# Kernel tuning notes

Measured on AMD Instinct MI355X. Metric: run time of the kernel, lower is better.

Reference implementation:

```python
import jax, jax.numpy as jnp
import numpy as np

N_EMBD = 1024
N_HEAD = 16
HEAD_DIM = N_EMBD // N_HEAD
INNER = 4 * N_EMBD
EPS = 1e-5


def setup_inputs() -> dict:
    key = jax.random.key(0)
    ks = jax.random.split(key, 13)
    s = lambda d: 1.0 / np.sqrt(d)
    return {
        "x": jax.random.normal(ks[0], (2, 2048, N_EMBD), jnp.float32),
        "ln1_g": jnp.ones((N_EMBD,), jnp.float32),
        "ln1_b": jnp.zeros((N_EMBD,), jnp.float32),
        "w_attn": jax.random.normal(ks[1], (N_EMBD, 3 * N_EMBD), jnp.float32) * s(N_EMBD),
        "b_attn": jnp.zeros((3 * N_EMBD,), jnp.float32),
        "w_proj": jax.random.normal(ks[2], (N_EMBD, N_EMBD), jnp.float32) * s(N_EMBD),
        "b_proj": jnp.zeros((N_EMBD,), jnp.float32),
        "ln2_g": jnp.ones((N_EMBD,), jnp.float32),
        "ln2_b": jnp.zeros((N_EMBD,), jnp.float32),
        "w_fc": jax.random.normal(ks[3], (N_EMBD, INNER), jnp.float32) * s(N_EMBD),
        "b_fc": jnp.zeros((INNER,), jnp.float32),
        "w_fc2": jax.random.normal(ks[4], (INNER, N_EMBD), jnp.float32) * s(INNER),
        "b_fc2": jnpp if False else jnp.zeros((N_EMBD,), jnp.float32),
    }


def _layernorm(x, g, b):
    mu = jnp.mean(x, axis=-1, keepdims=True)
    var = jnp.mean(jnp.square(x - mu), axis=-1, keepdims=True)
    return (x - mu) * jax.lax.rsqrt(var + EPS) * g + b


def _attention(x, w_attn, b_attn, w_proj, b_proj):
    B, T, C = x.shape
    qkv = x @ w_attn + b_attn                      # [B,T,3C]
    q, k, v = jnp.split(qkv, 3, axis=-1)
    q = q.reshape(B, T, N_HEAD, HEAD_DIM).transpose(0, 2, 1, 3)  # [B,H,T,D]
    k = k.reshape(B, T, N_HEAD, HEAD_DIM).transpose(0, 2, 1, 3)
    v = v.reshape(B, T, N_HEAD, HEAD_DIM).transpose(0, 2, 1, 3)
    scale = HEAD_DIM ** -0.5
    scores = jnp.einsum("bhqd,bhkd->bhqk", q, k) * scale         # [B,H,T,T]
    causal = jnp.triu(jnp.ones((T, T), jnp.bool_), k=1)
    scores = jnp.where(causal, -jnp.inf, scores)
    attn = jax.nn.softmax(scores, axis=-1)
    out = jnp.einsum("bhqk,bhkd->bhqd", attn, v)                 # [B,H,T,D]
    out = out.transpose(0, 2, 1, 3).reshape(B, T, C)
    return out @ w_proj + b_proj


def reference(x, ln1_g, ln1_b, w_attn, b_attn, w_proj, b_proj,
              ln2_g, ln2_b, w_fc, b_fc, w_fc2, b_fc2):
    h = x + _attention(_layernorm(x, ln1_g, ln1_b), w_attn, b_attn, w_proj, b_proj)
    m = _layernorm(h, ln2_g, ln2_b)
    m = jax.nn.gelu(m @ w_fc + b_fc, approximate=False) @ w_fc2 + b_fc2
    return h + m
```

## Files before the change

kernel.cpp:

```cpp
#include <hip/hip_runtime.h>

typedef unsigned short u16;
typedef unsigned int u32;
typedef short v8s __attribute__((ext_vector_type(8)));
typedef short v4s __attribute__((ext_vector_type(4)));
typedef float v4f __attribute__((ext_vector_type(4)));

__device__ __forceinline__ float b2f(u16 v) {
    return __uint_as_float(((u32)v) << 16);
}
__device__ __forceinline__ u16 f2b(float f) {
    u32 u = __float_as_uint(f);
    return (u16)((u + 0x7FFFu + ((u >> 16) & 1u)) >> 16);
}
__device__ __forceinline__ v4f mfma16(v8s a, v8s b, v4f c) {
    return __builtin_amdgcn_mfma_f32_16x16x32_bf16(a, b, c, 0, 0, 0);
}

__device__ __forceinline__ void gload_lds16(const u16* g, u16* l) {
    __builtin_amdgcn_global_load_lds((const __attribute__((address_space(1))) void*)g,
                                     (__attribute__((address_space(3))) void*)l, 16, 0, 0);
}

__global__ void detect_k(const void* x, int* flag) {
    __shared__ int cnt;
    if (threadIdx.x == 0) cnt = 0;
    __syncthreads();
    const u16* p = (const u16*)x;
    int bad = 0;
    for (int i = threadIdx.x; i < 4096; i += 256) {
        int e = (p[i] >> 7) & 0xFF;
        if (e != 0 && (e < 100 || e > 140)) bad++;
    }
    atomicAdd(&cnt, bad);
    __syncthreads();
    if (threadIdx.x == 0) *flag = (cnt > 256) ? 1 : 0;
}

__global__ void cvt_k(const void* __restrict__ src, u16* __restrict__ dst, int n,
                      const int* __restrict__ flag) {
    const int isf32 = *flag;
    for (int i = blockIdx.x * 256 + threadIdx.x; i < n; i += gridDim.x * 256)
        dst[i] = isf32 ? f2b(((const float*)src)[i]) : ((const u16*)src)[i];
}

struct P8 { const void* p[8]; };
__global__ void cvt_small_k(P8 src, u16* __restrict__ bb, const int* __restrict__ flag) {
    const int isf32 = *flag;
    const int len[8] = {3072, 1024, 4096, 1024, 1024, 1024, 1024, 1024};
    const int doff[8] = {0, 4096, 8192, 12288, 16384, 17408, 18432, 19456};
    int gi = blockIdx.x * 256 + threadIdx.x;
    int seg = 0, off = gi;
    while (seg < 7 && off >= len[seg]) { off -= len[seg]; seg++; }
    if (off < len[seg]) {
        const void* s = src.p[seg];
        bb[doff[seg] + off] = isf32 ? f2b(((const float*)s)[off]) : ((const u16*)s)[off];
    }
}

__global__ void transpose_k(const void* __restrict__ in, u16* __restrict__ out, int R, int C,
                            const int* __restrict__ flag) {
    __shared__ u16 t[32][33];
    const int isf32 = *flag;
    const int c0 = blockIdx.x * 32, r0 = blockIdx.y * 32;
    for (int i = threadIdx.y; i < 32; i += 8) {
        size_t idx = (size_t)(r0 + i) * C + c0 + threadIdx.x;
        t[i][threadIdx.x] = isf32 ? f2b(((const float*)in)[idx]) : ((const u16*)in)[idx];
    }
    __syncthreads();
    for (int i = threadIdx.y; i < 32; i += 8)
        out[(size_t)(c0 + i) * R + r0 + threadIdx.x] = t[threadIdx.x][i];
}

__global__ __launch_bounds__(256) void layernorm_k(const u16* __restrict__ x,
                                                   const u16* __restrict__ g,
                                                   const u16* __restrict__ bta,
                                                   u16* __restrict__ out) {
    const int wid = threadIdx.x >> 6, lane = threadIdx.x & 63;
    const size_t row = (size_t)blockIdx.x * 4 + wid;
    const u16* xr = x + row * 1024 + lane * 16;
    u16 v[16];
    *(uint4*)&v[0] = *(const uint4*)xr;
    *(uint4*)&v[8] = *(const uint4*)(xr + 8);
    float f[16], s = 0.f, sq = 0.f;
#pragma unroll
    for (int i = 0; i < 16; i++) { f[i] = b2f(v[i]); s += f[i]; sq += f[i] * f[i]; }
#pragma unroll
    for (int d = 1; d < 64; d <<= 1) { s += __shfl_xor(s, d, 64); sq += __shfl_xor(sq, d, 64); }
    const float mean = s * (1.f / 1024.f);
    const float var = sq * (1.f / 1024.f) - mean * mean;
    const float rstd = rsqrtf(var + 1e-5f);
    u16 gv[16], bv[16];
    *(uint4*)&gv[0] = *(const uint4*)(g + lane * 16);
    *(uint4*)&gv[8] = *(const uint4*)(g + lane * 16 + 8);
    *(uint4*)&bv[0] = *(const uint4*)(bta + lane * 16);
    *(uint4*)&bv[8] = *(const uint4*)(bta + lane * 16 + 8);
    u16 ov[16];
#pragma unroll
    for (int i = 0; i < 16; i++) ov[i] = f2b((f[i] - mean) * rstd * b2f(gv[i]) + b2f(bv[i]));
    u16* orow = out + row * 1024 + lane * 16;
    *(uint4*)orow = *(uint4*)&ov[0];
    *(uint4*)(orow + 8) = *(uint4*)&ov[8];
}

#define GEMM_STAGE(tk, buf)                                              \
    do {                                                                 \
        const int _k = (tk) << 5;                                        \
        gload_lds16(Ag + _k, &As[buf][0] + wid * 512);                   \
        gload_lds16(Ag + (size_t)64 * K + _k, &As[buf][2048] + wid * 512); \
        gload_lds16(Bg + _k, &Bs[buf][0] + wid * 512);                   \
        gload_lds16(Bg + (size_t)64 * K + _k, &Bs[buf][2048] + wid * 512); \
    } while (0)

__global__ __launch_bounds__(256) void gemm_bt_k(const u16* __restrict__ A,
                                                 const u16* __restrict__ Bt,
                                                 const u16* __restrict__ bias,
                                                 const u16* __restrict__ res,
                                                 void* __restrict__ C,
                                                 int M, int N, int K, int do_gelu,
                                                 const int* __restrict__ outf32) {
    __shared__ __align__(16) u16 As[3][4096];
    __shared__ __align__(16) u16 Bs[3][4096];
    const int tid = threadIdx.x;
    const int wid = tid >> 6, lane = tid & 63;
    const int lg = lane >> 4, lm = lane & 15;
    const int wr = wid >> 1, wc = wid & 1;
    const int nwg = gridDim.x * gridDim.y;
    const int orig = blockIdx.y * gridDim.x + blockIdx.x;
    const int wg = (orig & 7) * (nwg >> 3) + (orig >> 3);
    const int m0 = (wg / gridDim.x) * 128, n0 = (wg % gridDim.x) * 128;

    const v4f vzero = {0.f, 0.f, 0.f, 0.f};
    v4f acc[4][4];
#pragma unroll
    for (int i = 0; i < 4; i++)
#pragma unroll
        for (int j = 0; j < 4; j++) acc[i][j] = vzero;

    const int srow = tid >> 2;
    const int scol = (((tid & 3) ^ ((tid >> 3) & 3)) * 8);
    const u16* Ag = A + (size_t)(m0 + srow) * K + scol;
    const u16* Bg = Bt + (size_t)(n0 + srow) * K + scol;
    const int lgx = (lg ^ ((lm >> 1) & 3)) * 8;

    const int nt = K >> 5;
    GEMM_STAGE(0, 0);
    GEMM_STAGE(1, 1);
    for (int t = 0; t < nt; ++t) {
        const int cur = t % 3;
        if (t + 2 < nt) {
            GEMM_STAGE(t + 2, (t + 2) % 3);
            asm volatile("s_waitcnt vmcnt(8)" ::: "memory");
        } else if (t + 1 < nt) {
            asm volatile("s_waitcnt vmcnt(4)" ::: "memory");
        } else {
            asm volatile("s_waitcnt vmcnt(0)" ::: "memory");
        }
        __builtin_amdgcn_s_barrier();
        v8s af[4], bf[4];
#pragma unroll
        for (int i = 0; i < 4; i++)
            af[i] = *(const v8s*)&As[cur][(wr * 64 + i * 16 + lm) * 32 + lgx];
#pragma unroll
        for (int j = 0; j < 4; j++)
            bf[j] = *(const v8s*)&Bs[cur][(wc * 64 + j * 16 + lm) * 32 + lgx];
        __builtin_amdgcn_s_setprio(1);
#pragma unroll
        for (int i = 0; i < 4; i++)
#pragma unroll
            for (int j = 0; j < 4; j++)
                acc[i][j] = __builtin_amdgcn_mfma_f32_16x16x32_bf16(af[i], bf[j], acc[i][j], 0, 0, 0);
        __builtin_amdgcn_s_setprio(0);
        asm volatile("s_waitcnt lgkmcnt(0)" ::: "memory");
        __builtin_amdgcn_sched_barrier(0);
        __builtin_amdgcn_s_barrier();
    }

    const int of32 = outf32 ? *outf32 : 0;
#pragma unroll
    for (int i = 0; i < 4; i++) {
#pragma unroll
        for (int r = 0; r < 4; r++) {
            const int row = m0 + wr * 64 + i * 16 + lg * 4 + r;
            const size_t rb = (size_t)row * N;
#pragma unroll
            for (int j = 0; j < 4; j++) {
                const int col = n0 + wc * 64 + j * 16 + lm;
                float v = acc[i][j][r] + b2f(bias[col]);
                if (do_gelu) v = 0.5f * v * (1.0f + erff(v * 0.70710678118f));
                if (res) v += b2f(res[rb + col]);
                if (of32) ((float*)C)[rb + col] = v;
                else ((u16*)C)[rb + col] = f2b(v);
            }
        }
    }
}

#define ST256(LDSARR, P, tt, h)                                                  \
    do {                                                                         \
        const u16* _s = (P) + (size_t)((h) * 128) * K + (size_t)(tt) * 64;       \
        gload_lds16(_s, &LDSARR[(tt) & 1][h][0] + wv * 512);                     \
        gload_lds16(_s + (size_t)64 * K, &LDSARR[(tt) & 1][h][4096] + wv * 512); \
    } while (0)

#define MMROW(ii, x0, x1)                                   \
    acc[ii][0] = mfma16(x0, bfr[0][0], acc[ii][0]);         \
    acc[ii][0] = mfma16(x1, bfr[0][1], acc[ii][0]);         \
    acc[ii][1] = mfma16(x0, bfr[1][0], acc[ii][1]);         \
    acc[ii][1] = mfma16(x1, bfr[1][1], acc[ii][1]);         \
    acc[ii][2] = mfma16(x0, bfr[2][0], acc[ii][2]);         \
    acc[ii][2] = mfma16(x1, bfr[2][1], acc[ii][2]);         \
    acc[ii][3] = mfma16(x0, bfr[3][0], acc[ii][3]);         \
    acc[ii][3] = mfma16(x1, bfr[3][1], acc[ii][3]);

#define RD_A2(i0, i1)                                         \
    x0 = *(const v8s*)(ABase + (i0) * 1024 + offk0);          \
    x1 = *(const v8s*)(ABase + (i0) * 1024 + offk1);          \
    y0 = *(const v8s*)(ABase + (i1) * 1024 + offk0);          \
    y1 = *(const v8s*)(ABase + (i1) * 1024 + offk1);

__global__ __launch_bounds__(512, 2) void gemm256_k(const u16* __restrict__ A,
                                                    const u16* __restrict__ Bt,
                                                    const u16* __restrict__ bias,
                                                    const u16* __restrict__ res,
                                                    void* __restrict__ C,
                                                    int M, int N, int K, int do_gelu,
                                                    const int* __restrict__ outf32) {
    __shared__ __align__(16) u16 As[2][2][8192];
    __shared__ __align__(16) u16 Bs[2][2][8192];
    const int tid = threadIdx.x;
    const int wv = tid >> 6, lane = tid & 63;
    const int lg = lane >> 4, lm = lane & 15;
    const int wm = wv >> 2, wn = wv & 3;
    const int nwg = gridDim.x * gridDim.y;
    const int orig = blockIdx.y * gridDim.x + blockIdx.x;
    const int wg = (orig & 7) * (nwg >> 3) + (orig >> 3);
    const int m0 = (wg / gridDim.x) * 256, n0 = (wg % gridDim.x) * 256;

    const v4f vzero = {0.f, 0.f, 0.f, 0.f};
    v4f acc[8][4];
#pragma unroll
    for (int i = 0; i < 8; i++)
#pragma unroll
        for (int j = 0; j < 4; j++) acc[i][j] = vzero;

    const int trow = tid >> 3;
    const int csw = ((tid & 7) ^ (trow & 7)) * 8;
    const u16* Ap = A + (size_t)(m0 + trow) * K + csw;
    const u16* Bp = Bt + (size_t)(n0 + trow) * K + csw;
    const int offk0 = lm * 64 + ((lg ^ (lm & 7)) << 3);
    const int offk1 = offk0 ^ 32;

    const int NT = K >> 6;
    ST256(As, Ap, 0, 0); ST256(As, Ap, 0, 1);
    ST256(Bs, Bp, 0, 0); ST256(Bs, Bp, 0, 1);
    ST256(Bs, Bp, 1, 0); ST256(Bs, Bp, 1, 1);
    asm volatile("s_waitcnt vmcnt(4)" ::: "memory");
    __builtin_amdgcn_s_barrier();

    for (int t = 0; t < NT; ++t) {
        const int d = t & 1;
        const u16* ABase = &As[d][wm][0];
        const u16* BBase = &Bs[d][wn >> 1][(wn & 1) * 4096];
        v8s bfr[4][2];
        v8s x0, x1, y0, y1;
#pragma unroll
        for (int j = 0; j < 4; j++) {
            bfr[j][0] = *(const v8s*)(BBase + j * 1024 + offk0);
            bfr[j][1] = *(const v8s*)(BBase + j * 1024 + offk1);
        }
        RD_A2(0, 1)
        if (t + 1 < NT) { ST256(As, Ap, t + 1, 0); }
        __builtin_amdgcn_s_barrier();
        asm volatile("s_waitcnt lgkmcnt(0)" ::: "memory");
        __builtin_amdgcn_s_setprio(1);
        MMROW(0, x0, x1)
        MMROW(1, y0, y1)
        __builtin_amdgcn_s_setprio(0);
        __builtin_amdgcn_s_barrier();
        RD_A2(2, 3)
        if (t + 1 < NT) { ST256(As, Ap, t + 1, 1); }
        __builtin_amdgcn_s_barrier();
        asm volatile("s_waitcnt lgkmcnt(0)" ::: "memory");
        __builtin_amdgcn_s_setprio(1);
        MMROW(2, x0, x1)
        MMROW(3, y0, y1)
        __builtin_amdgcn_s_setprio(0);
        __builtin_amdgcn_s_barrier();
        RD_A2(4, 5)
        if (t + 2 < NT) { ST256(Bs, Bp, t + 2, 0); }
        __builtin_amdgcn_s_barrier();
        asm volatile("s_waitcnt lgkmcnt(0)" ::: "memory");
        __builtin_amdgcn_s_setprio(1);
        MMROW(4, x0, x1)
        MMROW(5, y0, y1)
        __builtin_amdgcn_s_setprio(0);
        __builtin_amdgcn_s_barrier();
        RD_A2(6, 7)
        if (t + 2 < NT) {
            ST256(Bs, Bp, t + 2, 1);
            asm volatile("s_waitcnt vmcnt(4)" ::: "memory");
        } else {
            asm volatile("s_waitcnt vmcnt(0)" ::: "memory");
        }
        __builtin_amdgcn_s_barrier();
        asm volatile("s_waitcnt lgkmcnt(0)" ::: "memory");
        __builtin_amdgcn_s_setprio(1);
        MMROW(6, x0, x1)
        MMROW(7, y0, y1)
        __builtin_amdgcn_s_setprio(0);
        __builtin_amdgcn_s_barrier();
    }

    const int of32 = outf32 ? *outf32 : 0;
#pragma unroll
    for (int i = 0; i < 8; i++) {
#pragma unroll
        for (int r = 0; r < 4; r++) {
            const int row = m0 + wm * 128 + i * 16 + lg * 4 + r;
            const size_t rb = (size_t)row * N;
#pragma unroll
            for (int j = 0; j < 4; j++) {
                const int col = n0 + wn * 64 + j * 16 + lm;
                float v = acc[i][j][r] + b2f(bias[col]);
                if (do_gelu) v = 0.5f * v * (1.0f + erff(v * 0.70710678118f));
                if (res) v += b2f(res[rb + col]);
                if (of32) ((float*)C)[rb + col] = v;
                else ((u16*)C)[rb + col] = f2b(v);
            }
        }
    }
}

__global__ __launch_bounds__(256) void gemm_qkv_k(const u16* __restrict__ A,
                                                  const u16* __restrict__ Bt,
                                                  const u16* __restrict__ bias,
                                                  u16* __restrict__ Qh,
                                                  u16* __restrict__ Kh,
                                                  u16* __restrict__ Vth) {
    __shared__ __align__(16) u16 As[3][4096];
    __shared__ __align__(16) u16 Bs[3][4096];
    const int tid = threadIdx.x;
    const int wid = tid >> 6, lane = tid & 63;
    const int lg = lane >> 4, lm = lane & 15;
    const int wr = wid >> 1, wc = wid & 1;
    const int nwg = gridDim.x * gridDim.y;
    const int orig = blockIdx.y * gridDim.x + blockIdx.x;
    const int wg = (orig & 7) * (nwg >> 3) + (orig >> 3);
    const int m0 = (wg / gridDim.x) * 128, n0 = (wg % gridDim.x) * 128;
    const int K = 1024;

    const v4f vzero = {0.f, 0.f, 0.f, 0.f};
    v4f acc[4][4];
#pragma unroll
    for (int i = 0; i < 4; i++)
#pragma unroll
        for (int j = 0; j < 4; j++) acc[i][j] = vzero;

    const int srow = tid >> 2;
    const int scol = (((tid & 3) ^ ((tid >> 3) & 3)) * 8);
    const u16* Ag = A + (size_t)(m0 + srow) * K + scol;
    const u16* Bg = Bt + (size_t)(n0 + srow) * K + scol;
    const int lgx = (lg ^ ((lm >> 1) & 3)) * 8;

    const int nt = K >> 5;
    GEMM_STAGE(0, 0);
    GEMM_STAGE(1, 1);
    for (int t = 0; t < nt; ++t) {
        const int cur = t % 3;
        if (t + 2 < nt) {
            GEMM_STAGE(t + 2, (t + 2) % 3);
            asm volatile("s_waitcnt vmcnt(8)" ::: "memory");
        } else if (t + 1 < nt) {
            asm volatile("s_waitcnt vmcnt(4)" ::: "memory");
        } else {
            asm volatile("s_waitcnt vmcnt(0)" ::: "memory");
        }
        __builtin_amdgcn_s_barrier();
        v8s af[4], bf[4];
#pragma unroll
        for (int i = 0; i < 4; i++)
            af[i] = *(const v8s*)&As[cur][(wr * 64 + i * 16 + lm) * 32 + lgx];
#pragma unroll
        for (int j = 0; j < 4; j++)
            bf[j] = *(const v8s*)&Bs[cur][(wc * 64 + j * 16 + lm) * 32 + lgx];
        __builtin_amdgcn_s_setprio(1);
#pragma unroll
        for (int i = 0; i < 4; i++)
#pragma unroll
            for (int j = 0; j < 4; j++)
                acc[i][j] = __builtin_amdgcn_mfma_f32_16x16x32_bf16(af[i], bf[j], acc[i][j], 0, 0, 0);
        __builtin_amdgcn_s_setprio(0);
        asm volatile("s_waitcnt lgkmcnt(0)" ::: "memory");
        __builtin_amdgcn_sched_barrier(0);
        __builtin_amdgcn_s_barrier();
    }

    const int which = n0 >> 10;
    const int h = ((n0 & 1023) >> 6) + wc;
    if (which < 2) {
        u16* dst = which ? Kh : Qh;
        const float qsc = which ? 1.0f : 0.18033688011f;
#pragma unroll
        for (int i = 0; i < 4; i++) {
#pragma unroll
            for (int r = 0; r < 4; r++) {
                const int row = m0 + wr * 64 + i * 16 + lg * 4 + r;
                const int b = row >> 11, t = row & 2047;
                const size_t rb = ((size_t)(b * 16 + h) * 2048 + t) * 64;
#pragma unroll
                for (int j = 0; j < 4; j++) {
                    float v = (acc[i][j][r] + b2f(bias[n0 + wc * 64 + j * 16 + lm])) * qsc;
                    dst[rb + j * 16 + lm] = f2b(v);
                }
            }
        }
    } else {
#pragma unroll
        for (int i = 0; i < 4; i++) {
            const int t0 = m0 + wr * 64 + i * 16 + lg * 4;
            const int b = t0 >> 11, tt = t0 & 2047;
            const int w = tt & 31;
            const int pos = (tt & ~31) + ((w & 15) >> 2) * 8 + ((w >> 4) & 1) * 4;
#pragma unroll
            for (int j = 0; j < 4; j++) {
                const int d = j * 16 + lm;
                const float bv_ = b2f(bias[n0 + wc * 64 + j * 16 + lm]);
                u16 pk[4];
#pragma unroll
                for (int r = 0; r < 4; r++) pk[r] = f2b(acc[i][j][r] + bv_);
                *(v4s*)&Vth[((size_t)(b * 16 + h) * 64 + d) * 2048 + pos] = *(const v4s*)pk;
            }
        }
    }
}

__global__ __launch_bounds__(256, 4) void attn10_k(const u16* __restrict__ Qh,
                                                   const u16* __restrict__ Kh,
                                                   const u16* __restrict__ Vth,
                                                   u16* __restrict__ out) {
    __shared__ __align__(16) u16 Ks[2][4096];
    __shared__ __align__(16) u16 Vs[2][4096];
    const int tid = threadIdx.x;
    const int wid = tid >> 6, lane = tid & 63;
    const int lg = lane >> 4, lm = lane & 15;
    const int i = blockIdx.x;
    const int q = i >> 8, s = i & 255;
    const int bh = s & 31;
    const int g8 = s >> 5;
    const int g = (q == 0) ? g8 : (q == 1) ? (15 - g8) : (q == 2) ? (16 + g8) : (31 - g8);
    const int q0 = g * 64 + wid * 16;
    const int qrow_l = q0 + lm;
    const size_t qkb = (size_t)bh * 2048;
    const v4f vzero = {0.f, 0.f, 0.f, 0.f};
    const int nch = g + 1;

    const int r0 = tid >> 3;
    const int colp = ((tid & 7) * 16) ^ ((r0 & 7) << 4);
    const u16* Ksrc0 = Kh + (qkb + r0) * 64 + (colp >> 1);
    const u16* Ksrc1 = Ksrc0 + 32 * 64;
    const u16* Vsrc0 = Vth + ((size_t)bh * 64 + r0) * 2048 + (colp >> 1);
    const u16* Vsrc1 = Vsrc0 + (size_t)32 * 2048;
    const int wslot = wid * 512;

    const int xorv = (lm & 7) << 4;
    const int ro1 = (lm * 128 + ((lg * 16) ^ xorv)) >> 1;
    const int ro2 = (lm * 128 + (((lg * 16) + 64) ^ xorv)) >> 1;

    v8s aq[2];
    {
        const u16* qp = Qh + (qkb + q0 + lm) * 64 + lg * 8;
        aq[0] = *(const v8s*)qp;
        aq[1] = *(const v8s*)(qp + 32);
    }
    float l_run = 0.f;
    v4f o[4];
#pragma unroll
    for (int dt = 0; dt < 4; dt++) o[dt] = vzero;

    gload_lds16(Ksrc0, &Ks[0][0] + wslot);
    gload_lds16(Ksrc1, &Ks[0][2048] + wslot);
    gload_lds16(Vsrc0, &Vs[0][0] + wslot);
    gload_lds16(Vsrc1, &Vs[0][2048] + wslot);

    for (int ci = 0; ci < nch; ++ci) {
        const int cur = ci & 1;
        if (ci + 1 < nch) {
            const u16* kc = Ksrc0 + (ci + 1) * 4096;
            const u16* vc = Vsrc0 + (ci + 1) * 64;
            gload_lds16(kc, &Ks[cur ^ 1][0] + wslot);
            gload_lds16(kc + 32 * 64, &Ks[cur ^ 1][2048] + wslot);
            gload_lds16(vc, &Vs[cur ^ 1][0] + wslot);
            gload_lds16(vc + (size_t)32 * 2048, &Vs[cur ^ 1][2048] + wslot);
            asm volatile("s_waitcnt vmcnt(4)" ::: "memory");
        } else {
            asm volatile("s_waitcnt vmcnt(0)" ::: "memory");
        }
        __builtin_amdgcn_s_barrier();

        const u16* KB = &Ks[cur][0];
        const u16* VB = &Vs[cur][0];
        const int k0 = ci << 6;
        v4f sacc[4];
        __builtin_amdgcn_s_setprio(1);
#pragma unroll
        for (int kt = 0; kt < 4; kt++) {
            v8s klo = *(const v8s*)(KB + kt * 1024 + ro1);
            v8s khi = *(const v8s*)(KB + kt * 1024 + ro2);
            sacc[kt] = __builtin_amdgcn_mfma_f32_16x16x32_bf16(klo, aq[0], vzero, 0, 0, 0);
            sacc[kt] = __builtin_amdgcn_mfma_f32_16x16x32_bf16(khi, aq[1], sacc[kt], 0, 0, 0);
        }
        __builtin_amdgcn_s_setprio(0);
        float p[16];
        if (ci == nch - 1) {
#pragma unroll
            for (int kt = 0; kt < 4; kt++)
#pragma unroll
                for (int r = 0; r < 4; r++) {
                    float v = sacc[kt][r];
                    v = (k0 + kt * 16 + lg * 4 + r > qrow_l) ? -200.f : v;
                    p[kt * 4 + r] = exp2f(v);
                }
        } else {
#pragma unroll
            for (int kt = 0; kt < 4; kt++)
#pragma unroll
                for (int r = 0; r < 4; r++) p[kt * 4 + r] = exp2f(sacc[kt][r]);
        }
        float ls = 0.f;
#pragma unroll
        for (int e = 0; e < 16; e++) ls += p[e];
        l_run += ls;
        u32 pk[8];
#pragma unroll
        for (int j = 0; j < 8; j++) {
            u32 lo = __float_as_uint(p[j * 2]) + 0x8000u;
            u32 hi = __float_as_uint(p[j * 2 + 1]) + 0x8000u;
            pk[j] = __builtin_amdgcn_perm(hi, lo, 0x07060302u);
        }
        v8s B0, B1;
        ((u32*)&B0)[0] = pk[0]; ((u32*)&B0)[1] = pk[1];
        ((u32*)&B0)[2] = pk[2]; ((u32*)&B0)[3] = pk[3];
        ((u32*)&B1)[0] = pk[4]; ((u32*)&B1)[1] = pk[5];
        ((u32*)&B1)[2] = pk[6]; ((u32*)&B1)[3] = pk[7];
        __builtin_amdgcn_s_setprio(1);
#pragma unroll
        for (int dt = 0; dt < 4; dt++) {
            v8s vlo = *(const v8s*)(VB + dt * 1024 + ro1);
            v8s vhi = *(const v8s*)(VB + dt * 1024 + ro2);
            o[dt] = __builtin_amdgcn_mfma_f32_16x16x32_bf16(vlo, B0, o[dt], 0, 0, 0);
            o[dt] = __builtin_amdgcn_mfma_f32_16x16x32_bf16(vhi, B1, o[dt], 0, 0, 0);
        }
        __builtin_amdgcn_s_setprio(0);
        asm volatile("s_waitcnt lgkmcnt(0)" ::: "memory");
        __builtin_amdgcn_sched_barrier(0);
        __builtin_amdgcn_s_barrier();
    }
    l_run += __shfl_xor(l_run, 16, 64);
    l_run += __shfl_xor(l_run, 32, 64);
    const int b = bh >> 4, h = bh & 15;
    const float inv = 1.0f / l_run;
    const size_t rowb = ((size_t)b * 2048 + q0 + lm) * 1024 + h * 64;
#pragma unroll
    for (int dt = 0; dt < 4; dt++) {
        u16 pk2[4];
#pragma unroll
        for (int r = 0; r < 4; r++) pk2[r] = f2b(o[dt][r] * inv);
        *(v4s*)&out[rowb + dt * 16 + lg * 4] = *(const v4s*)pk2;
    }
}

extern "C" void kernel_launch(void* const* d_in, const int* in_sizes, int n_in,
                              void* d_out, int out_size, void* d_ws, size_t ws_size,
                              hipStream_t stream) {
    const void* x      = d_in[0];
    const void* ln1_g  = d_in[1];
    const void* ln1_b  = d_in[2];
    const void* w_attn = d_in[3];
    const void* b_attn = d_in[4];
    const void* w_proj = d_in[5];
    const void* b_proj = d_in[6];
    const void* ln2_g  = d_in[7];
    const void* ln2_b  = d_in[8];
    const void* w_fc   = d_in[9];
    const void* b_fc   = d_in[10];
    const void* w_fc2  = d_in[11];
    const void* b_fc2  = d_in[12];

    u16* ws = (u16*)d_ws;
    const size_t Mi = 1u << 20;
    u16* xb       = ws;
    u16* ln_buf   = ws + 4 * Mi;
    u16* h_buf    = ws + 8 * Mi;
    u16* wT_attn  = ws + 12 * Mi;
    u16* wT_proj  = ws + 15 * Mi;
    u16* wT_fc    = ws + 16 * Mi;
    u16* wT_fc2   = ws + 20 * Mi;
    u16* bb       = ws + 24 * Mi;
    u16* bb_attn = bb, *bb_proj = bb + 4096, *bb_fc = bb + 8192, *bb_fc2 = bb + 12288;
    u16* gsmall   = bb + 16384;
    u16* g_ln1g = gsmall, *g_ln1b = gsmall + 1024, *g_ln2g = gsmall + 2048, *g_ln2b = gsmall + 3072;
    int* flag     = (int*)(bb + 24576);
    u16* Qh       = ws + 25 * Mi;
    u16* Kh       = ws + 29 * Mi;
    u16* Vth      = ws + 33 * Mi;
    u16* attn_buf = ws + 37 * Mi;
    u16* fc_buf   = ws + 25 * Mi;

    detect_k<<<1, 256, 0, stream>>>(x, flag);

    cvt_k<<<4096, 256, 0, stream>>>(x, xb, 4 * Mi, flag);
    P8 smalls;
    smalls.p[0] = b_attn; smalls.p[1] = b_proj; smalls.p[2] = b_fc; smalls.p[3] = b_fc2;
    smalls.p[4] = ln1_g;  smalls.p[5] = ln1_b;  smalls.p[6] = ln2_g; smalls.p[7] = ln2_b;
    cvt_small_k<<<52, 256, 0, stream>>>(smalls, bb, flag);

    dim3 tb(32, 8);
    transpose_k<<<dim3(96, 32), tb, 0, stream>>>(w_attn, wT_attn, 1024, 3072, flag);
    transpose_k<<<dim3(32, 32), tb, 0, stream>>>(w_proj, wT_proj, 1024, 1024, flag);
    transpose_k<<<dim3(128, 32), tb, 0, stream>>>(w_fc, wT_fc, 1024, 4096, flag);
    transpose_k<<<dim3(32, 128), tb, 0, stream>>>(w_fc2, wT_fc2, 4096, 1024, flag);

    layernorm_k<<<1024, 256, 0, stream>>>(xb, g_ln1g, g_ln1b, ln_buf);
    gemm_qkv_k<<<dim3(24, 32), 256, 0, stream>>>(ln_buf, wT_attn, bb_attn, Qh, Kh, Vth);
    attn10_k<<<1024, 256, 0, stream>>>(Qh, Kh, Vth, attn_buf);
    gemm_bt_k<<<dim3(8, 32), 256, 0, stream>>>(attn_buf, wT_proj, bb_proj, xb, h_buf,
                                               4096, 1024, 1024, 0, nullptr);
    layernorm_k<<<1024, 256, 0, stream>>>(h_buf, g_ln2g, g_ln2b, ln_buf);
    gemm256_k<<<dim3(16, 16), 512, 0, stream>>>(ln_buf, wT_fc, bb_fc, nullptr, fc_buf,
                                                4096, 4096, 1024, 1, nullptr);
    gemm_bt_k<<<dim3(8, 32), 256, 0, stream>>>(fc_buf, wT_fc2, bb_fc2, h_buf, d_out,
                                               4096, 1024, 4096, 0, flag);
}
```

Baseline: 455.1 us.

## Split-K the FC2 GEMM into two fp32 partials with a fused reduce epilogue

Replaces the single FC2 GEMM launch (256 tiles with full K=4096) with a split-K kernel that runs 512 workgroups, each covering half of K with a 3-stage LDS pipeline. Each half writes fp32 partial results into reused workspace regions. A separate reduce kernel then adds the two partials, the bias and the residual, and writes the output in fp32 or bf16. The aim is more workgroups per CU for better latency hiding. The cost is extra fp32 partial traffic and one more kernel launch.

```diff
diff --git a/kernel.cpp b/kernel.cpp
--- a/kernel.cpp
+++ b/kernel.cpp
@@ -193,6 +193,111 @@
                 else ((u16*)C)[rb + col] = f2b(v);
             }
         }
+    }
+}
+
+__global__ __launch_bounds__(256) void gemm_sk_k(const u16* __restrict__ A,
+                                                 const u16* __restrict__ Bt,
+                                                 float* __restrict__ P0,
+                                                 float* __restrict__ P1,
+                                                 int N, int K) {
+    __shared__ __align__(16) u16 As[3][4096];
+    __shared__ __align__(16) u16 Bs[3][4096];
+    const int tid = threadIdx.x;
+    const int wid = tid >> 6, lane = tid & 63;
+    const int lg = lane >> 4, lm = lane & 15;
+    const int wr = wid >> 1, wc = wid & 1;
+    const int z = blockIdx.z;
+    const int KS = K >> 1;
+    const int nwg = gridDim.x * gridDim.y;
+    const int orig = blockIdx.y * gridDim.x + blockIdx.x;
+    const int wg = (orig & 7) * (nwg >> 3) + (orig >> 3);
+    const int m0 = (wg / gridDim.x) * 128, n0 = (wg % gridDim.x) * 128;
+
+    const v4f vzero = {0.f, 0.f, 0.f, 0.f};
+    v4f acc[4][4];
+#pragma unroll
+    for (int i = 0; i < 4; i++)
+#pragma unroll
+        for (int j = 0; j < 4; j++) acc[i][j] = vzero;
+
+    const int srow = tid >> 2;
+    const int scol = (((tid & 3) ^ ((tid >> 3) & 3)) * 8);
+    const u16* Ag = A + (size_t)(m0 + srow) * K + z * KS + scol;
+    const u16* Bg = Bt + (size_t)(n0 + srow) * K + z * KS + scol;
+    const int lgx = (lg ^ ((lm >> 1) & 3)) * 8;
+
+    const int nt = KS >> 5;
+    GEMM_STAGE(0, 0);
+    GEMM_STAGE(1, 1);
+    for (int t = 0; t < nt; ++t) {
+        const int cur = t % 3;
+        if (t + 2 < nt) {
+            GEMM_STAGE(t + 2, (t + 2) % 3);
+            asm volatile("s_waitcnt vmcnt(8)" ::: "memory");
+        } else if (t + 1 < nt) {
+            asm volatile("s_waitcnt vmcnt(4)" ::: "memory");
+        } else {
+            asm volatile("s_waitcnt vmcnt(0)" ::: "memory");
+        }
+        __builtin_amdgcn_s_barrier();
+        v8s af[4], bf[4];
+#pragma unroll
+        for (int i = 0; i < 4; i++)
+            af[i] = *(const v8s*)&As[cur][(wr * 64 + i * 16 + lm) * 32 + lgx];
+#pragma unroll
+        for (int j = 0; j < 4; j++)
+            bf[j] = *(const v8s*)&Bs[cur][(wc * 64 + j * 16 + lm) * 32 + lgx];
+        __builtin_amdgcn_s_setprio(1);
+#pragma unroll
+        for (int i = 0; i < 4; i++)
+#pragma unroll
+            for (int j = 0; j < 4; j++)
+                acc[i][j] = __builtin_amdgcn_mfma_f32_16x16x32_bf16(af[i], bf[j], acc[i][j], 0, 0, 0);
+        __builtin_amdgcn_s_setprio(0);
+        asm volatile("s_waitcnt lgkmcnt(0)" ::: "memory");
+        __builtin_amdgcn_sched_barrier(0);
+        __builtin_amdgcn_s_barrier();
+    }
+
+    float* P = z ? P1 : P0;
+#pragma unroll
+    for (int i = 0; i < 4; i++) {
+#pragma unroll
+        for (int r = 0; r < 4; r++) {
+            const int row = m0 + wr * 64 + i * 16 + lg * 4 + r;
+            const size_t rb = (size_t)row * N;
+#pragma unroll
+            for (int j = 0; j < 4; j++) {
+                const int col = n0 + wc * 64 + j * 16 + lm;
+                P[rb + col] = acc[i][j][r];
+            }
+        }
+    }
+}
+
+__global__ __launch_bounds__(256) void fc2red_k(const float* __restrict__ P0,
+                                                const float* __restrict__ P1,
+                                                const u16* __restrict__ bias,
+                                                const u16* __restrict__ res,
+                                                void* __restrict__ out,
+                                                const int* __restrict__ outf32) {
+    const int i = (blockIdx.x * 256 + threadIdx.x) * 4;
+    const int col = i & 1023;
+    float4 a = *(const float4*)(P0 + i);
+    float4 b = *(const float4*)(P1 + i);
+    v4s rv = *(const v4s*)(res + i);
+    v4s bv = *(const v4s*)(bias + col);
+    float v0 = a.x + b.x + b2f(bv[0]) + b2f(rv[0]);
+    float v1 = a.y + b.y + b2f(bv[1]) + b2f(rv[1]);
+    float v2 = a.z + b.z + b2f(bv[2]) + b2f(rv[2]);
+    float v3 = a.w + b.w + b2f(bv[3]) + b2f(rv[3]);
+    if (*outf32) {
+        float4 o = {v0, v1, v2, v3};
+        *(float4*)((float*)out + i) = o;
+    } else {
+        u16 pk[4] = {f2b(v0), f2b(v1), f2b(v2), f2b(v3)};
+        *(v4s*)((u16*)out + i) = *(const v4s*)pk;
     }
 }
 
@@ -606,6 +711,8 @@
     u16* Vth      = ws + 33 * Mi;
     u16* attn_buf = ws + 37 * Mi;
     u16* fc_buf   = ws + 25 * Mi;
+    float* P0f    = (float*)ws;
+    float* P1f    = (float*)(ws + 12 * Mi);
 
     detect_k<<<1, 256, 0, stream>>>(x, flag);
 
@@ -629,6 +736,6 @@
     layernorm_k<<<1024, 256, 0, stream>>>(h_buf, g_ln2g, g_ln2b, ln_buf);
     gemm256_k<<<dim3(16, 16), 512, 0, stream>>>(ln_buf, wT_fc, bb_fc, nullptr, fc_buf,
                                                 4096, 4096, 1024, 1, nullptr);
-    gemm_bt_k<<<dim3(8, 32), 256, 0, stream>>>(fc_buf, wT_fc2, bb_fc2, h_buf, d_out,
-                                               4096, 1024, 4096, 0, flag);
-}
+    gemm_sk_k<<<dim3(8, 32, 2), 256, 0, stream>>>(fc_buf, wT_fc2, P0f, P1f, 1024, 4096);
+    fc2red_k<<<4096, 256, 0, stream>>>(P0f, P1f, bb_fc2, h_buf, d_out, flag);
+}
```

Result: faster. 424.1 us (-6.8%).
